# Kernel optimization log

Measured on AMD Instinct MI355X. Metric: run time of the kernel, lower is better.

The kernel has to match this reference:

```python
import jax, jax.numpy as jnp
import numpy as np

N = 1048576
C = 128

def setup_inputs() -> dict:
    key = jax.random.key(0)
    k1, k2 = jax.random.split(key)
    # probabilities must be positive for log; uniform in (1e-6, 1)
    predicts = jax.random.uniform(k1, (N, C), dtype=jnp.float32, minval=1e-6, maxval=1.0)
    labels = jax.random.randint(k2, (N,), 0, C, dtype=jnp.int64)
    return {"predicts": predicts, "labels": labels}

def reference(predicts, labels):
    # loss = -(1/N) * sum_i log(predicts[i, labels[i]])
    labels = labels.reshape(-1)
    picked = jnp.take_along_axis(predicts, labels[:, None], axis=1)[:, 0]  # [N]
    return -jnp.mean(jnp.log(picked))
```

## Files before the change

### kernel.cpp

```cpp
#include <hip/hip_runtime.h>

#define BLOCK 256
#define C 128
#define F4_PER_ROW (C / 4)
#define GRID_CAP 2048

__global__ __launch_bounds__(BLOCK) void MultiCrossEntropyLoss_kernel(
    const float4* __restrict__ predicts4,
    const int*    __restrict__ labels,
    float*        __restrict__ out,
    int total4, float inv_n)
{
    const int tid    = blockIdx.x * BLOCK + threadIdx.x;
    const int stride = gridDim.x * BLOCK;
    const int slot   = tid & 31;

    float s = 0.0f;
    #pragma unroll 4
    for (int idx = tid; idx < total4; idx += stride) {
        const float4 v   = predicts4[idx];
        const int    lab = labels[idx >> 5];
        if ((lab >> 2) == slot) {
            const float x01 = (lab & 1) ? v.y : v.x;
            const float x23 = (lab & 1) ? v.w : v.z;
            const float x   = (lab & 2) ? x23 : x01;
            s += __logf(x);
        }
    }

    #pragma unroll
    for (int off = 32; off > 0; off >>= 1)
        s += __shfl_down(s, off, 64);

    __shared__ float wave_sums[BLOCK / 64];
    const int lane = threadIdx.x & 63;
    const int wv   = threadIdx.x >> 6;
    if (lane == 0) wave_sums[wv] = s;
    __syncthreads();

    if (threadIdx.x == 0) {
        float bs = wave_sums[0] + wave_sums[1] + wave_sums[2] + wave_sums[3];
        atomicAdd(out, -bs * inv_n);
    }
}

extern "C" void kernel_launch(void* const* d_in, const int* in_sizes, int n_in,
                              void* d_out, int out_size, void* d_ws, size_t ws_size,
                              hipStream_t stream) {
    const float* predicts = (const float*)d_in[0];
    const int*   labels   = (const int*)d_in[1];
    float*       out      = (float*)d_out;
    const int n = in_sizes[1];

    hipMemsetAsync(d_out, 0, sizeof(float), stream);

    const int total4 = n * F4_PER_ROW;
    int grid = (total4 + BLOCK - 1) / BLOCK;
    if (grid > GRID_CAP) grid = GRID_CAP;
    MultiCrossEntropyLoss_kernel<<<grid, BLOCK, 0, stream>>>(
        (const float4*)predicts, labels, out, total4, 1.0f / (float)n);
}
```

Measured before the change: 653.7 us.

## Assign fixed row tiles per block with labels staged in LDS

Replaces the grid-stride loop with fixed 512-row tiles per block, giving a grid of about 2048 blocks. Each block first stages its labels into shared memory instead of re-reading a label per float4 from global memory. The main loop runs unrolled and branch-free, with two accumulators and a predicated log, so loads can be issued back to back. This computes a log for every element, not only the matched one, and adds a __syncthreads before streaming.

Measured after the change: 673.7 us. +3.1%, slower.

```diff
diff --git a/kernel.cpp b/kernel.cpp
--- a/kernel.cpp
+++ b/kernel.cpp
@@ -1,38 +1,67 @@
 #include <hip/hip_runtime.h>
 
 #define BLOCK 256
-#define C 128
-#define F4_PER_ROW (C / 4)
-#define GRID_CAP 2048
+#define RPB   512
+#define C     128
+#define F4_PER_ROW   (C / 4)
+#define F4_PER_BLOCK (RPB * F4_PER_ROW)
+#define ITERS        (F4_PER_BLOCK / BLOCK)
 
 __global__ __launch_bounds__(BLOCK) void MultiCrossEntropyLoss_kernel(
     const float4* __restrict__ predicts4,
     const int*    __restrict__ labels,
     float*        __restrict__ out,
-    int total4, float inv_n)
+    int n, float inv_n)
 {
-    const int tid    = blockIdx.x * BLOCK + threadIdx.x;
-    const int stride = gridDim.x * BLOCK;
-    const int slot   = tid & 31;
+    __shared__ int   lds_lab[RPB];
+    __shared__ float wave_sums[BLOCK / 64];
 
-    float s = 0.0f;
-    #pragma unroll 4
-    for (int idx = tid; idx < total4; idx += stride) {
-        const float4 v   = predicts4[idx];
-        const int    lab = labels[idx >> 5];
-        if ((lab >> 2) == slot) {
+    const int row0 = blockIdx.x * RPB;
+    const int rows = min(RPB, n - row0);
+
+    for (int r = threadIdx.x; r < rows; r += BLOCK)
+        lds_lab[r] = labels[row0 + r];
+    __syncthreads();
+
+    const int slot  = threadIdx.x & 31;
+    const int rbase = threadIdx.x >> 5;
+    const float4* p = predicts4 + (size_t)row0 * F4_PER_ROW + threadIdx.x;
+
+    float s0 = 0.0f, s1 = 0.0f;
+
+    if (rows == RPB) {
+        #pragma unroll 8
+        for (int k = 0; k < ITERS; ++k) {
+            const float4 v   = p[k * BLOCK];
+            const int    lab = lds_lab[rbase + (k << 3)];
             const float x01 = (lab & 1) ? v.y : v.x;
             const float x23 = (lab & 1) ? v.w : v.z;
             const float x   = (lab & 2) ? x23 : x01;
-            s += __logf(x);
+            const float lg  = __logf(x);
+            const float c   = ((lab >> 2) == slot) ? lg : 0.0f;
+            if (k & 1) s1 += c; else s0 += c;
+        }
+    } else {
+        for (int k = 0; k < ITERS; ++k) {
+            const int idx = threadIdx.x + k * BLOCK;
+            const int r   = idx >> 5;
+            if (r < rows) {
+                const float4 v   = p[k * BLOCK];
+                const int    lab = lds_lab[r];
+                const float x01 = (lab & 1) ? v.y : v.x;
+                const float x23 = (lab & 1) ? v.w : v.z;
+                const float x   = (lab & 2) ? x23 : x01;
+                if ((lab >> 2) == slot) s0 += __logf(x);
+            }
         }
     }
+
+    float s = s0 + s1;
 
     #pragma unroll
     for (int off = 32; off > 0; off >>= 1)
         s += __shfl_down(s, off, 64);
 
-    __shared__ float wave_sums[BLOCK / 64];
     const int lane = threadIdx.x & 63;
     const int wv   = threadIdx.x >> 6;
     if (lane == 0) wave_sums[wv] = s;
@@ -54,9 +83,7 @@
 
     hipMemsetAsync(d_out, 0, sizeof(float), stream);
 
-    const int total4 = n * F4_PER_ROW;
-    int grid = (total4 + BLOCK - 1) / BLOCK;
-    if (grid > GRID_CAP) grid = GRID_CAP;
+    const int grid = (n + RPB - 1) / RPB;
     MultiCrossEntropyLoss_kernel<<<grid, BLOCK, 0, stream>>>(
-        (const float4*)predicts, labels, out, total4, 1.0f / (float)n);
+        (const float4*)predicts, labels, out, n, 1.0f / (float)n);
 }
```
